# Performance work log

Measured on AMD Instinct MI355X. Metric: run time of the kernel, lower is better.

The kernel has to match this reference:

```python
import jax, jax.numpy as jnp
import numpy as np

INPUT = 256
HIDDEN = 1024
OUTPUT = 256
B, T = 64, 512


def setup_inputs() -> dict:
    key = jax.random.key(0)
    ks = jax.random.split(key, 7)
    s_ih = 1.0 / np.sqrt(INPUT)
    s_hh = 1.0 / np.sqrt(HIDDEN)
    return {
        "input_seq": jax.random.normal(ks[0], (B, T, INPUT), jnp.float32),
        "W_ih": jax.random.uniform(ks[1], (INPUT, 4 * HIDDEN), jnp.float32, -s_ih, s_ih),
        "W_hh": jax.random.uniform(ks[2], (HIDDEN, 4 * HIDDEN), jnp.float32, -s_hh, s_hh),
        "b_ih": jax.random.uniform(ks[3], (4 * HIDDEN,), jnp.float32, -s_hh, s_hh),
        "b_hh": jax.random.uniform(ks[4], (4 * HIDDEN,), jnp.float32, -s_hh, s_hh),
        "W_out": jax.random.uniform(ks[5], (HIDDEN, OUTPUT), jnp.float32, -s_hh, s_hh),
        "b_out": jax.random.uniform(ks[6], (OUTPUT,), jnp.float32, -s_hh, s_hh),
    }


def _lstm_last_hidden(x, W_ih, W_hh, b_ih, b_hh):
    Bsz = x.shape[0]
    H = W_hh.shape[0]
    # Precompute input-side gate projections for all timesteps: [T, B, 4H]
    x_t = jnp.einsum('bti,ih->tbh', x, W_ih) + b_ih + b_hh

    def step(carry, xg):
        h, c = carry
        gates = xg + h @ W_hh  # [B, 4H]
        i, f, g, o = jnp.split(gates, 4, axis=-1)
        i = jax.nn.sigmoid(i)
        f = jax.nn.sigmoid(f)
        g = jnp.tanh(g)
        o = jax.nn.sigmoid(o)
        c = f * c + i * g
        h = o * jnp.tanh(c)
        return (h, c), None

    h0 = jnp.zeros((Bsz, H), x.dtype)
    c0 = jnp.zeros((Bsz, H), x.dtype)
    (h_last, _), _ = jax.lax.scan(step, (h0, c0), x_t)
    return h_last


def reference(input_seq, W_ih, W_hh, b_ih, b_hh, W_out, b_out):
    h_last = _lstm_last_hidden(input_seq, W_ih, W_hh, b_ih, b_hh)  # [B, H]
    return h_last @ W_out + b_out  # [B, OUTPUT]
```

## Files before the change

### kernel.cpp

```cpp
#include <hip/hip_runtime.h>
#include <hip/hip_bf16.h>
#include <cstdint>

#define HIDDEN 1024
#define INPUT  256
#define BATCH  64
#define TSTEPS 512
#define NGCOL  4096
#define KTOT   1280
#define HBUFN  65536
#define FSTRIDE 16

typedef __attribute__((ext_vector_type(8))) short bf16x8;
typedef __attribute__((ext_vector_type(4))) float f32x4;
typedef unsigned long long u64;
typedef unsigned int u32;

__device__ inline short f2bs(float f) {
    union { __hip_bfloat16 h; short s; } u;
    u.h = __float2bfloat16(f);
    return u.s;
}
__device__ inline unsigned short f2bu(float f) {
    union { __hip_bfloat16 h; unsigned short s; } u;
    u.h = __float2bfloat16(f);
    return u.s;
}

__global__ __launch_bounds__(256) void build_wt(
    const float* __restrict__ Whh, const float* __restrict__ Wih,
    __hip_bfloat16* __restrict__ Wt)
{
    int t = blockIdx.x * 256 + threadIdx.x;
    int col = t & 4095;
    int k0  = (t >> 12) * 16;
    __hip_bfloat16 tmp[16];
    if (k0 < HIDDEN) {
        #pragma unroll
        for (int i = 0; i < 16; ++i)
            tmp[i] = __float2bfloat16(Whh[(size_t)(k0 + i) * NGCOL + col]);
    } else {
        #pragma unroll
        for (int i = 0; i < 16; ++i)
            tmp[i] = __float2bfloat16(Wih[(size_t)(k0 - HIDDEN + i) * NGCOL + col]);
    }
    #pragma unroll
    for (int i = 0; i < 16; ++i)
        Wt[(size_t)col * KTOT + k0 + i] = tmp[i];
}

__global__ __launch_bounds__(256) void init_state(
    const float* __restrict__ bih, const float* __restrict__ bhh,
    float* __restrict__ bias, u32* __restrict__ hbuf, u32* __restrict__ cnt)
{
    int i = blockIdx.x * 256 + threadIdx.x;
    if (i < NGCOL) bias[i] = bih[i] + bhh[i];
    hbuf[i] = 0u;
    if (i < 256 * FSTRIDE) cnt[i] = 0u;
}

__global__ __launch_bounds__(512, 2) void lstm_persist(
    const __hip_bfloat16* __restrict__ Wt,
    const float* __restrict__ x,
    u32* __restrict__ hbuf,
    float* __restrict__ hf,
    const float* __restrict__ bias,
    u32* __restrict__ cnt)
{
    __shared__ float pbuf[8][1025];

    const int tid  = threadIdx.x;
    const int wg   = blockIdx.x;
    const int bg   = wg >> 6;
    const int cg   = wg & 63;
    const int wave = tid >> 6;
    const int lane = tid & 63;
    const int l15  = lane & 15;
    const int l4   = lane >> 4;
    const int b0   = bg * 16;
    const int n0   = cg * 16;

    const __hip_bfloat16* wrow = Wt + (size_t)(n0 + l15) * KTOT;
    bf16x8 w[5][4];
    #pragma unroll
    for (int c5 = 0; c5 < 5; ++c5) {
        const int kk = (wave + c5 * 8) * 32 + l4 * 8;
        #pragma unroll
        for (int g = 0; g < 4; ++g)
            w[c5][g] = *(const bf16x8*)(wrow + (size_t)g * 1024 * KTOT + kk);
    }

    const int br = tid >> 4;
    const int hc = tid & 15;
    float creg = 0.f;
    float bi = 0.f, bfr = 0.f, bgg = 0.f, bo = 0.f;
    if (tid < 256) {
        bi  = bias[0 * 1024 + n0 + hc];
        bfr = bias[1 * 1024 + n0 + hc];
        bgg = bias[2 * 1024 + n0 + hc];
        bo  = bias[3 * 1024 + n0 + hc];
    }

    const int hoff = (b0 + l15) * HIDDEN + wave * 32 + l4 * 8;
    const float* xrow = x + ((size_t)(b0 + l15) * TSTEPS) * INPUT + wave * 32 + l4 * 8;

    const int pj = 2 * wave + (lane & 1) + 16 * ((lane >> 1) & 3);
    const u32* myflag = cnt + (size_t)(bg * 64 + pj) * FSTRIDE;

    for (int t = 0; t < TSTEPS; ++t) {
        const u32* hb = hbuf + (t & 1) * HBUFN;
        u32*       ho = hbuf + ((t + 1) & 1) * HBUFN;

        bf16x8 afx;
        {
            const float* xf = xrow + (size_t)t * INPUT;
            float4 pa = *(const float4*)(xf);
            float4 pb = *(const float4*)(xf + 4);
            afx[0] = f2bs(pa.x); afx[1] = f2bs(pa.y); afx[2] = f2bs(pa.z); afx[3] = f2bs(pa.w);
            afx[4] = f2bs(pb.x); afx[5] = f2bs(pb.y); afx[6] = f2bs(pb.z); afx[7] = f2bs(pb.w);
        }
        f32x4 a0 = {0.f, 0.f, 0.f, 0.f};
        f32x4 a1 = a0, a2 = a0, a3 = a0;
        a0 = __builtin_amdgcn_mfma_f32_16x16x32_bf16(afx, w[4][0], a0, 0, 0, 0);
        a1 = __builtin_amdgcn_mfma_f32_16x16x32_bf16(afx, w[4][1], a1, 0, 0, 0);
        a2 = __builtin_amdgcn_mfma_f32_16x16x32_bf16(afx, w[4][2], a2, 0, 0, 0);
        a3 = __builtin_amdgcn_mfma_f32_16x16x32_bf16(afx, w[4][3], a3, 0, 0, 0);

        for (;;) {
            u32 f = __hip_atomic_load(myflag, __ATOMIC_RELAXED, __HIP_MEMORY_SCOPE_AGENT);
            if (__all(f >= (u32)t)) break;
            __builtin_amdgcn_s_sleep(1);
        }

        u64 hq[4][4];
        {
            const u64 want = ((u64)(u32)t << 16) | ((u64)(u32)t << 48);
            const u64 mask = 0xFFFF0000FFFF0000ull;
            for (;;) {
                u64 bad = 0;
                #pragma unroll
                for (int c5 = 0; c5 < 4; ++c5) {
                    const u64* hp = (const u64*)(hb + hoff + c5 * 256);
                    #pragma unroll
                    for (int q = 0; q < 4; ++q) {
                        hq[c5][q] = __hip_atomic_load(hp + q, __ATOMIC_RELAXED,
                                                      __HIP_MEMORY_SCOPE_AGENT);
                        bad |= (hq[c5][q] ^ want) & mask;
                    }
                }
                if (__all(bad == 0)) break;
                __builtin_amdgcn_s_sleep(1);
            }
        }
        bf16x8 afh[4];
        #pragma unroll
        for (int c5 = 0; c5 < 4; ++c5) {
            union { u32 p[4]; bf16x8 v; } u;
            #pragma unroll
            for (int q = 0; q < 4; ++q) {
                const u64 d = hq[c5][q];
                u.p[q] = (u32)(d & 0xFFFFu) | ((u32)(d >> 32) << 16);
            }
            afh[c5] = u.v;
        }

        #pragma unroll
        for (int c5 = 0; c5 < 4; ++c5) {
            a0 = __builtin_amdgcn_mfma_f32_16x16x32_bf16(afh[c5], w[c5][0], a0, 0, 0, 0);
            a1 = __builtin_amdgcn_mfma_f32_16x16x32_bf16(afh[c5], w[c5][1], a1, 0, 0, 0);
            a2 = __builtin_amdgcn_mfma_f32_16x16x32_bf16(afh[c5], w[c5][2], a2, 0, 0, 0);
            a3 = __builtin_amdgcn_mfma_f32_16x16x32_bf16(afh[c5], w[c5][3], a3, 0, 0, 0);
        }

        float* pw = &pbuf[wave][0];
        #pragma unroll
        for (int r = 0; r < 4; ++r) {
            const int row = l4 * 4 + r;
            pw[(0 * 16 + row) * 16 + l15] = a0[r];
            pw[(1 * 16 + row) * 16 + l15] = a1[r];
            pw[(2 * 16 + row) * 16 + l15] = a2[r];
            pw[(3 * 16 + row) * 16 + l15] = a3[r];
        }
        __syncthreads();

        if (tid < 256) {
            float gi = bi, gf = bfr, gg = bgg, go = bo;
            #pragma unroll
            for (int w8 = 0; w8 < 8; ++w8) {
                const float* p = &pbuf[w8][0];
                gi += p[(0 * 16 + br) * 16 + hc];
                gf += p[(1 * 16 + br) * 16 + hc];
                gg += p[(2 * 16 + br) * 16 + hc];
                go += p[(3 * 16 + br) * 16 + hc];
            }
            const float i_ = 1.f / (1.f + __expf(-gi));
            const float f_ = 1.f / (1.f + __expf(-gf));
            const float g_ = tanhf(gg);
            const float o_ = 1.f / (1.f + __expf(-go));
            creg = f_ * creg + i_ * g_;
            const float h = o_ * tanhf(creg);
            if (t == TSTEPS - 1) {
                hf[(b0 + br) * HIDDEN + n0 + hc] = h;
            } else {
                const u32 val = ((u32)(t + 1) << 16) | (u32)f2bu(h);
                __hip_atomic_store(ho + (b0 + br) * HIDDEN + n0 + hc, val,
                                   __ATOMIC_RELAXED, __HIP_MEMORY_SCOPE_AGENT);
            }
        }
        if (t == TSTEPS - 1) break;
        __syncthreads();

        if (tid == 0)
            __hip_atomic_store(cnt + (size_t)wg * FSTRIDE, (u32)(t + 1),
                               __ATOMIC_RELAXED, __HIP_MEMORY_SCOPE_AGENT);
    }
}

__global__ __launch_bounds__(256) void out_proj(
    const float* __restrict__ hf, const float* __restrict__ Wout,
    const float* __restrict__ bout, float* __restrict__ out)
{
    const int b  = blockIdx.x;
    const int oc = threadIdx.x;
    const float* hb = hf + (size_t)b * HIDDEN;
    float a0 = 0.f, a1 = 0.f, a2 = 0.f, a3 = 0.f;
    for (int k = 0; k < HIDDEN; k += 4) {
        a0 += hb[k + 0] * Wout[(size_t)(k + 0) * 256 + oc];
        a1 += hb[k + 1] * Wout[(size_t)(k + 1) * 256 + oc];
        a2 += hb[k + 2] * Wout[(size_t)(k + 2) * 256 + oc];
        a3 += hb[k + 3] * Wout[(size_t)(k + 3) * 256 + oc];
    }
    out[b * 256 + oc] = (a0 + a1) + (a2 + a3) + bout[oc];
}

extern "C" void kernel_launch(void* const* d_in, const int* in_sizes, int n_in,
                              void* d_out, int out_size, void* d_ws, size_t ws_size,
                              hipStream_t stream)
{
    const float* x    = (const float*)d_in[0];
    const float* Wih  = (const float*)d_in[1];
    const float* Whh  = (const float*)d_in[2];
    const float* bih  = (const float*)d_in[3];
    const float* bhh  = (const float*)d_in[4];
    const float* Wout = (const float*)d_in[5];
    const float* bout = (const float*)d_in[6];
    float* out = (float*)d_out;

    char* ws = (char*)d_ws;
    size_t off = 0;
    auto alloc = [&](size_t bytes) -> void* {
        void* p = ws + off;
        off = (off + bytes + 255) & ~(size_t)255;
        return p;
    };
    __hip_bfloat16* Wt = (__hip_bfloat16*)alloc((size_t)NGCOL * KTOT * 2);
    u32*   hbuf = (u32*)alloc((size_t)2 * HBUFN * 4);
    float* bias = (float*)alloc((size_t)NGCOL * 4);
    float* hf   = (float*)alloc((size_t)BATCH * HIDDEN * 4);
    u32*   cnt  = (u32*)alloc((size_t)256 * FSTRIDE * 4);

    build_wt<<<1280, 256, 0, stream>>>(Whh, Wih, Wt);
    init_state<<<512, 256, 0, stream>>>(bih, bhh, bias, hbuf, cnt);
    lstm_persist<<<256, 512, 0, stream>>>(Wt, x, hbuf, hf, bias, cnt);
    out_proj<<<64, 256, 0, stream>>>(hf, Wout, bout, out);
}
```

Measured before the change: 2.881 ms.

## Move gate weights out of registers into LDS and per-step global reloads

After: 2.883 ms. No clear change (+0.1%).

```diff
diff --git a/kernel.cpp b/kernel.cpp
--- a/kernel.cpp
+++ b/kernel.cpp
@@ -68,6 +68,7 @@
     u32* __restrict__ cnt)
 {
     __shared__ float pbuf[8][1025];
+    __shared__ __attribute__((aligned(16))) short wlds[2][5][512][8];
 
     const int tid  = threadIdx.x;
     const int wg   = blockIdx.x;
@@ -81,13 +82,13 @@
     const int n0   = cg * 16;
 
     const __hip_bfloat16* wrow = Wt + (size_t)(n0 + l15) * KTOT;
-    bf16x8 w[5][4];
+
     #pragma unroll
     for (int c5 = 0; c5 < 5; ++c5) {
         const int kk = (wave + c5 * 8) * 32 + l4 * 8;
-        #pragma unroll
-        for (int g = 0; g < 4; ++g)
-            w[c5][g] = *(const bf16x8*)(wrow + (size_t)g * 1024 * KTOT + kk);
+        *(bf16x8*)&wlds[0][c5][tid][0] = *(const bf16x8*)(wrow + kk);
+        *(bf16x8*)&wlds[1][c5][tid][0] =
+            *(const bf16x8*)(wrow + (size_t)1024 * KTOT + kk);
     }
 
     const int br = tid >> 4;
@@ -111,6 +112,19 @@
         const u32* hb = hbuf + (t & 1) * HBUFN;
         u32*       ho = hbuf + ((t + 1) & 1) * HBUFN;
 
+        bf16x8 w2[5], w3[5];
+        #pragma unroll
+        for (int c5 = 0; c5 < 5; ++c5) {
+            const int kk = (wave + c5 * 8) * 32 + l4 * 8;
+            w2[c5] = *(const bf16x8*)(wrow + (size_t)2048 * KTOT + kk);
+            w3[c5] = *(const bf16x8*)(wrow + (size_t)3072 * KTOT + kk);
+        }
+        #pragma unroll
+        for (int c5 = 0; c5 < 5; ++c5) {
+            asm volatile("" : "+v"(w2[c5]));
+            asm volatile("" : "+v"(w3[c5]));
+        }
+
         bf16x8 afx;
         {
             const float* xf = xrow + (size_t)t * INPUT;
@@ -121,10 +135,12 @@
         }
         f32x4 a0 = {0.f, 0.f, 0.f, 0.f};
         f32x4 a1 = a0, a2 = a0, a3 = a0;
-        a0 = __builtin_amdgcn_mfma_f32_16x16x32_bf16(afx, w[4][0], a0, 0, 0, 0);
-        a1 = __builtin_amdgcn_mfma_f32_16x16x32_bf16(afx, w[4][1], a1, 0, 0, 0);
-        a2 = __builtin_amdgcn_mfma_f32_16x16x32_bf16(afx, w[4][2], a2, 0, 0, 0);
-        a3 = __builtin_amdgcn_mfma_f32_16x16x32_bf16(afx, w[4][3], a3, 0, 0, 0);
+        a0 = __builtin_amdgcn_mfma_f32_16x16x32_bf16(
+                 afx, *(const bf16x8*)&wlds[0][4][tid][0], a0, 0, 0, 0);
+        a1 = __builtin_amdgcn_mfma_f32_16x16x32_bf16(
+                 afx, *(const bf16x8*)&wlds[1][4][tid][0], a1, 0, 0, 0);
+        a2 = __builtin_amdgcn_mfma_f32_16x16x32_bf16(afx, w2[4], a2, 0, 0, 0);
+        a3 = __builtin_amdgcn_mfma_f32_16x16x32_bf16(afx, w3[4], a3, 0, 0, 0);
 
         for (;;) {
             u32 f = __hip_atomic_load(myflag, __ATOMIC_RELAXED, __HIP_MEMORY_SCOPE_AGENT);
@@ -166,10 +182,12 @@
 
         #pragma unroll
         for (int c5 = 0; c5 < 4; ++c5) {
-            a0 = __builtin_amdgcn_mfma_f32_16x16x32_bf16(afh[c5], w[c5][0], a0, 0, 0, 0);
-            a1 = __builtin_amdgcn_mfma_f32_16x16x32_bf16(afh[c5], w[c5][1], a1, 0, 0, 0);
-            a2 = __builtin_amdgcn_mfma_f32_16x16x32_bf16(afh[c5], w[c5][2], a2, 0, 0, 0);
-            a3 = __builtin_amdgcn_mfma_f32_16x16x32_bf16(afh[c5], w[c5][3], a3, 0, 0, 0);
+            a0 = __builtin_amdgcn_mfma_f32_16x16x32_bf16(
+                     afh[c5], *(const bf16x8*)&wlds[0][c5][tid][0], a0, 0, 0, 0);
+            a1 = __builtin_amdgcn_mfma_f32_16x16x32_bf16(
+                     afh[c5], *(const bf16x8*)&wlds[1][c5][tid][0], a1, 0, 0, 0);
+            a2 = __builtin_amdgcn_mfma_f32_16x16x32_bf16(afh[c5], w2[c5], a2, 0, 0, 0);
+            a3 = __builtin_amdgcn_mfma_f32_16x16x32_bf16(afh[c5], w3[c5], a3, 0, 0, 0);
         }
 
         float* pw = &pbuf[wave][0];
```
